# Kernel tuning notes

Measured on AMD Instinct MI355X. Metric: run time of the kernel, lower is better.

## Reference

```python
import jax, jax.numpy as jnp
import numpy as np

N, E, H = 40000, 640000, 128
EPS = 1e-5

def _bn(x, gamma, beta):
    # BatchNorm1d training-mode forward: batch mean / biased variance over axis 0
    mu = jnp.mean(x, axis=0)
    var = jnp.mean((x - mu) ** 2, axis=0)
    return (x - mu) * jax.lax.rsqrt(var + EPS) * gamma + beta


def setup_inputs() -> dict:
    key = jax.random.key(0)
    ks = jax.random.split(key, 12)
    s = 1.0 / np.sqrt(H)
    return {
        "x_feat": jax.random.normal(ks[0], (N, H), jnp.float32),
        "edge_attr": jax.random.normal(ks[1], (E, H), jnp.float32),
        "bases": jax.random.normal(ks[2], (E, H), jnp.float32),
        "src": jax.random.randint(ks[3], (E,), 0, N, jnp.int32),
        "dst": jax.random.randint(ks[4], (E,), 0, N, jnp.int32),
        "W1": jax.random.uniform(ks[5], (H, H), jnp.float32, -s, s),
        "b1": jnp.zeros((H,), jnp.float32),
        "W2": jax.random.uniform(ks[6], (H, H), jnp.float32, -s, s),
        "b2": jnp.zeros((H,), jnp.float32),
        "g1": jnp.ones((H,), jnp.float32),
        "be1": jnp.zeros((H,), jnp.float32),
        "W3": jax.random.uniform(ks[7], (H, H), jnp.float32, -s, s),
        "b3": jnp.zeros((H,), jnp.float32),
        "g2": jnp.ones((H,), jnp.float32),
        "be2": jnpp_zeros if False else jnp.zeros((H,), jnp.float32),
    }


def reference(x_feat, edge_attr, bases, src, dst,
              W1, b1, W2, b2, g1, be1, W3, b3, g2, be2):
    n_nodes = x_feat.shape[0]
    # edge gather-add: pos_e = x[src] + e
    pos_e = x_feat[src] + edge_attr                       # [E, H]
    # pre_ffn (Linear + exact GELU) then elementwise scale by bases
    v = jax.nn.gelu(pos_e @ W1.T + b1, approximate=False) * bases  # [E, H]
    # scatter-sum aggregation to destination nodes
    aggr = jax.ops.segment_sum(v, dst, num_segments=n_nodes)       # [N, H]
    # ffn: Linear -> BN -> GELU -> Linear -> BN -> GELU
    h = _bn(aggr @ W2.T + b2, g1, be1)
    h = jax.nn.gelu(h, approximate=False)
    h = _bn(h @ W3.T + b3, g2, be2)
    return jax.nn.gelu(h, approximate=False)
```

## Files before the change

### kernel.cpp

```cpp
#include <hip/hip_runtime.h>
#include <cmath>

#define H 128
#define EPS 1e-5f

typedef __attribute__((ext_vector_type(8))) __bf16 bf16x8;
typedef __attribute__((ext_vector_type(4))) float f32x4;
typedef __attribute__((ext_vector_type(2))) float f32x2;
typedef __attribute__((ext_vector_type(4))) unsigned short u16x4;
typedef __attribute__((ext_vector_type(8))) unsigned short u16x8;
typedef __attribute__((ext_vector_type(4))) int i32x4;

__device__ __forceinline__ float gelu_fast(float x) {
    float t2 = -1.5957691216057308f * fmaf(0.044715f * x * x, x, x);
    return x * __builtin_amdgcn_rcpf(1.0f + __expf(t2));
}

__device__ __forceinline__ unsigned short f2bfu(float f) {
    __bf16 h = (__bf16)f;
    return __builtin_bit_cast(unsigned short, h);
}

__global__ __launch_bounds__(256) void zero_kernel(int* __restrict__ p, int n4)
{
    int i = blockIdx.x * blockDim.x + threadIdx.x;
    const int stride = gridDim.x * blockDim.x;
    i32x4 z = {0, 0, 0, 0};
    for (; i < n4; i += stride)
        reinterpret_cast<i32x4*>(p)[i] = z;
}

__global__ __launch_bounds__(256) void hist_kernel(const int* __restrict__ dst,
                                                   int* __restrict__ cnt, int E)
{
    int i = blockIdx.x * blockDim.x + threadIdx.x;
    const int stride = gridDim.x * blockDim.x;
    for (; i < E; i += stride) atomicAdd(&cnt[dst[i]], 1);
}

__global__ __launch_bounds__(1024) void scan_kernel(const int* __restrict__ cnt,
                                                    int* __restrict__ offs,
                                                    int Nn, int E)
{
    __shared__ int part[1024];
    const int t = threadIdx.x;
    const int CH = (Nn + 1023) / 1024;
    const int base = t * CH;
    int s = 0;
    for (int i = 0; i < CH; ++i) {
        int idx = base + i;
        if (idx < Nn) s += cnt[idx];
    }
    part[t] = s;
    __syncthreads();
    for (int d = 1; d < 1024; d <<= 1) {
        int v = (t >= d) ? part[t - d] : 0;
        __syncthreads();
        part[t] += v;
        __syncthreads();
    }
    int run = (t > 0) ? part[t - 1] : 0;
    for (int i = 0; i < CH; ++i) {
        int idx = base + i;
        if (idx < Nn) {
            offs[idx] = run;
            run += cnt[idx];
        }
    }
    if (t == 0) offs[Nn] = E;
}

__global__ __launch_bounds__(256) void scatter_perm(const int* __restrict__ dst,
                                                    const int* __restrict__ offs,
                                                    int* __restrict__ cur2,
                                                    int* __restrict__ perm, int E)
{
    int i = blockIdx.x * blockDim.x + threadIdx.x;
    const int stride = gridDim.x * blockDim.x;
    for (; i < E; i += stride) {
        int n = dst[i];
        int p = offs[n] + atomicAdd(&cur2[n], 1);
        perm[p] = i;
    }
}

__global__ __launch_bounds__(256) void fused_edge(
    const float* __restrict__ x, const float* __restrict__ ea,
    const int* __restrict__ src, const float* __restrict__ W1,
    const float* __restrict__ b1, unsigned short* __restrict__ gbuf, int E)
{
    __shared__ __align__(16) unsigned short alds[64 * 128];

    const int tid = threadIdx.x;
    const int w = tid >> 6, l = tid & 63, lg = l >> 4, lr = l & 15;

    bf16x8 wf[2][4];
    f32x4 b1v[2];
#pragma unroll
    for (int ni = 0; ni < 2; ++ni) {
        int row = w * 32 + ni * 16 + lr;
#pragma unroll
        for (int kk = 0; kk < 4; ++kk) {
            const float* p = W1 + row * H + kk * 32 + lg * 8;
            u16x8 tt;
#pragma unroll
            for (int i = 0; i < 8; ++i) tt[i] = f2bfu(p[i]);
            wf[ni][kk] = __builtin_bit_cast(bf16x8, tt);
        }
        b1v[ni] = *reinterpret_cast<const f32x4*>(b1 + w * 32 + ni * 16 + lg * 4);
    }

    const int e0 = blockIdx.x * 64;

#pragma unroll
    for (int it = 0; it < 8; ++it) {
        const int gch = it * 256 + tid;
        const int row = gch >> 5;
        const int c16 = gch & 31;
        const int er = e0 + row;
        const int ec = er < E ? er : E - 1;
        const int s = src[ec];
        f32x4 a = *reinterpret_cast<const f32x4*>(ea + (long)ec * H + c16 * 4);
        f32x4 b = *reinterpret_cast<const f32x4*>(x + (long)s * H + c16 * 4);
        u16x4 o;
#pragma unroll
        for (int j = 0; j < 4; ++j) o[j] = f2bfu(a[j] + b[j]);
        const int col = c16 * 4;
        const int scol = col ^ ((row & 7) << 3);
        *reinterpret_cast<u16x4*>(&alds[row * 128 + scol]) = o;
    }
    __syncthreads();

#pragma unroll
    for (int s = 0; s < 4; ++s) {
        const int arow = s * 16 + lr;
        const int aswz = (arow & 7) << 3;
        bf16x8 af[4];
#pragma unroll
        for (int kk = 0; kk < 4; ++kk)
            af[kk] = __builtin_bit_cast(bf16x8,
                *reinterpret_cast<const u16x8*>(&alds[arow * 128 + ((kk * 32 + lg * 8) ^ aswz)]));
        const int es = e0 + s * 16 + lr;
#pragma unroll
        for (int ni = 0; ni < 2; ++ni) {
            f32x4 a4 = {0.f, 0.f, 0.f, 0.f};
#pragma unroll
            for (int kk = 0; kk < 4; ++kk)
                a4 = __builtin_amdgcn_mfma_f32_16x16x32_bf16(wf[ni][kk], af[kk], a4, 0, 0, 0);
            if (es < E) {
                u16x4 o;
#pragma unroll
                for (int r = 0; r < 4; ++r)
                    o[r] = f2bfu(gelu_fast(a4[r] + b1v[ni][r]));
                *reinterpret_cast<u16x4*>(gbuf + (size_t)es * H + w * 32 + ni * 16 + lg * 4) = o;
            }
        }
    }
}

__global__ __launch_bounds__(256) void aggregate_kernel(
    const unsigned short* __restrict__ gbuf, const float* __restrict__ bases,
    const int* __restrict__ perm, const int* __restrict__ offs,
    float* __restrict__ aggr, int Nn, int E)
{
    const int wv = threadIdx.x >> 6, lane = threadIdx.x & 63;
    const int n = blockIdx.x * 4 + wv;
    if (n >= Nn) return;
    const int lo = offs[n], hi = offs[n + 1];
    float a0 = 0.f, a1 = 0.f;
    int i = lo;
    for (; i + 3 < hi; i += 4) {
        int e0 = perm[i], e1 = perm[i + 1], e2 = perm[i + 2], e3 = perm[i + 3];
        e0 = (unsigned)e0 < (unsigned)E ? e0 : 0;
        e1 = (unsigned)e1 < (unsigned)E ? e1 : 0;
        e2 = (unsigned)e2 < (unsigned)E ? e2 : 0;
        e3 = (unsigned)e3 < (unsigned)E ? e3 : 0;
        unsigned u0 = *reinterpret_cast<const unsigned*>(gbuf + (size_t)e0 * H + lane * 2);
        unsigned u1 = *reinterpret_cast<const unsigned*>(gbuf + (size_t)e1 * H + lane * 2);
        unsigned u2 = *reinterpret_cast<const unsigned*>(gbuf + (size_t)e2 * H + lane * 2);
        unsigned u3 = *reinterpret_cast<const unsigned*>(gbuf + (size_t)e3 * H + lane * 2);
        f32x2 b0 = *reinterpret_cast<const f32x2*>(bases + (size_t)e0 * H + lane * 2);
        f32x2 b1_ = *reinterpret_cast<const f32x2*>(bases + (size_t)e1 * H + lane * 2);
        f32x2 b2 = *reinterpret_cast<const f32x2*>(bases + (size_t)e2 * H + lane * 2);
        f32x2 b3 = *reinterpret_cast<const f32x2*>(bases + (size_t)e3 * H + lane * 2);
        a0 += __builtin_bit_cast(float, u0 << 16) * b0[0]
            + __builtin_bit_cast(float, u1 << 16) * b1_[0]
            + __builtin_bit_cast(float, u2 << 16) * b2[0]
            + __builtin_bit_cast(float, u3 << 16) * b3[0];
        a1 += __builtin_bit_cast(float, u0 & 0xffff0000u) * b0[1]
            + __builtin_bit_cast(float, u1 & 0xffff0000u) * b1_[1]
            + __builtin_bit_cast(float, u2 & 0xffff0000u) * b2[1]
            + __builtin_bit_cast(float, u3 & 0xffff0000u) * b3[1];
    }
    for (; i < hi; ++i) {
        int e = perm[i];
        e = (unsigned)e < (unsigned)E ? e : 0;
        unsigned u0 = *reinterpret_cast<const unsigned*>(gbuf + (size_t)e * H + lane * 2);
        f32x2 b0 = *reinterpret_cast<const f32x2*>(bases + (size_t)e * H + lane * 2);
        a0 += __builtin_bit_cast(float, u0 << 16) * b0[0];
        a1 += __builtin_bit_cast(float, u0 & 0xffff0000u) * b0[1];
    }
    f32x2 o = {a0, a1};
    *reinterpret_cast<f32x2*>(aggr + (size_t)n * H + lane * 2) = o;
}

template <bool PRE>
__global__ __launch_bounds__(256) void node_gemm(
    const float* __restrict__ A, const float* __restrict__ W,
    const float* __restrict__ bias, const float* __restrict__ scl,
    const float* __restrict__ shf, float* __restrict__ Y,
    float* __restrict__ csum, float* __restrict__ cssq, int Nn)
{
    __shared__ __align__(16) unsigned short alds[64 * 128];

    const int tid = threadIdx.x;
    const int w = tid >> 6, l = tid & 63, lg = l >> 4, lr = l & 15;
    const int er = tid >> 2, q = tid & 3;
    const int r0 = blockIdx.x * 64;

    bf16x8 bf[2][4];
    float bv[2];
#pragma unroll
    for (int n = 0; n < 2; ++n) {
        int row = w * 32 + n * 16 + lr;
        bv[n] = bias[row];
#pragma unroll
        for (int kk = 0; kk < 4; ++kk) {
            const float* p = W + row * H + kk * 32 + lg * 8;
            u16x8 t;
#pragma unroll
            for (int i = 0; i < 8; ++i) t[i] = f2bfu(p[i]);
            bf[n][kk] = __builtin_bit_cast(bf16x8, t);
        }
    }

    {
        int rr = r0 + er;
        int rc = rr < Nn ? rr : Nn - 1;
        const f32x4* pa = reinterpret_cast<const f32x4*>(A + (long)rc * H + q * 32);
        const int swz = (er & 7) << 3;
#pragma unroll
        for (int i = 0; i < 8; ++i) {
            f32x4 v = pa[i];
            if constexpr (PRE) {
                f32x4 sc = *reinterpret_cast<const f32x4*>(scl + q * 32 + i * 4);
                f32x4 sh = *reinterpret_cast<const f32x4*>(shf + q * 32 + i * 4);
#pragma unroll
                for (int c = 0; c < 4; ++c) v[c] = gelu_fast(v[c] * sc[c] + sh[c]);
            }
            u16x4 o;
            o[0] = f2bfu(v[0]);
            o[1] = f2bfu(v[1]);
            o[2] = f2bfu(v[2]);
            o[3] = f2bfu(v[3]);
            int col = q * 32 + i * 4;
            *reinterpret_cast<u16x4*>(&alds[er * 128 + (col ^ swz)]) = o;
        }
    }
    __syncthreads();

    float ps[2] = {0.f, 0.f}, ps2[2] = {0.f, 0.f};
#pragma unroll
    for (int m = 0; m < 4; ++m) {
        const int arow = m * 16 + lr;
        const int aswz = (arow & 7) << 3;
        bf16x8 af[4];
#pragma unroll
        for (int kk = 0; kk < 4; ++kk)
            af[kk] = __builtin_bit_cast(bf16x8,
                *reinterpret_cast<const u16x8*>(&alds[arow * 128 + ((kk * 32 + lg * 8) ^ aswz)]));
#pragma unroll
        for (int n = 0; n < 2; ++n) {
            f32x4 a4 = {0.f, 0.f, 0.f, 0.f};
#pragma unroll
            for (int kk = 0; kk < 4; ++kk)
                a4 = __builtin_amdgcn_mfma_f32_16x16x32_bf16(af[kk], bf[n][kk], a4, 0, 0, 0);
            const int j = w * 32 + n * 16 + lr;
#pragma unroll
            for (int r = 0; r < 4; ++r) {
                int rr = r0 + m * 16 + lg * 4 + r;
                if (rr < Nn) {
                    float z = a4[r] + bv[n];
                    Y[(long)rr * H + j] = z;
                    ps[n] += z;
                    ps2[n] += z * z;
                }
            }
        }
    }
#pragma unroll
    for (int n = 0; n < 2; ++n) {
        float s = ps[n];
        s += __shfl_xor(s, 16);
        s += __shfl_xor(s, 32);
        float s2 = ps2[n];
        s2 += __shfl_xor(s2, 16);
        s2 += __shfl_xor(s2, 32);
        if (lg == 0) {
            int j = w * 32 + n * 16 + lr;
            atomicAdd(&csum[j], s);
            atomicAdd(&cssq[j], s2);
        }
    }
}

__global__ void finalize_bn(const float* __restrict__ csum, const float* __restrict__ cssq,
                            const float* __restrict__ g, const float* __restrict__ be,
                            float* __restrict__ scl, float* __restrict__ shf, float invN)
{
    int j = threadIdx.x;
    float mu = csum[j] * invN;
    float var = fmaxf(cssq[j] * invN - mu * mu, 0.f);
    float s = g[j] * rsqrtf(var + EPS);
    scl[j] = s;
    shf[j] = be[j] - mu * s;
}

__global__ __launch_bounds__(256) void final_gelu(
    const float* __restrict__ Y2, const float* __restrict__ scl,
    const float* __restrict__ shf, float* __restrict__ out, long n4)
{
    long i = (long)blockIdx.x * blockDim.x + threadIdx.x;
    const long stride = (long)gridDim.x * blockDim.x;
    for (; i < n4; i += stride) {
        f32x4 v = reinterpret_cast<const f32x4*>(Y2)[i];
        int c4 = (int)(i & 31);
        f32x4 sc = reinterpret_cast<const f32x4*>(scl)[c4];
        f32x4 sh = reinterpret_cast<const f32x4*>(shf)[c4];
        f32x4 o;
#pragma unroll
        for (int c = 0; c < 4; ++c) o[c] = gelu_fast(v[c] * sc[c] + sh[c]);
        reinterpret_cast<f32x4*>(out)[i] = o;
    }
}

extern "C" void kernel_launch(void* const* d_in, const int* in_sizes, int n_in,
                              void* d_out, int out_size, void* d_ws, size_t ws_size,
                              hipStream_t stream) {
    const float* x     = (const float*)d_in[0];
    const float* ea    = (const float*)d_in[1];
    const float* bases = (const float*)d_in[2];
    const int*   src   = (const int*)d_in[3];
    const int*   dst   = (const int*)d_in[4];
    const float* W1    = (const float*)d_in[5];
    const float* b1    = (const float*)d_in[6];
    const float* W2    = (const float*)d_in[7];
    const float* b2    = (const float*)d_in[8];
    const float* g1    = (const float*)d_in[9];
    const float* be1   = (const float*)d_in[10];
    const float* W3    = (const float*)d_in[11];
    const float* b3    = (const float*)d_in[12];
    const float* g2    = (const float*)d_in[13];
    const float* be2   = (const float*)d_in[14];

    const int N = in_sizes[0] / H;
    const int E = in_sizes[1] / H;

    float* ws    = (float*)d_ws;
    float* aggr  = ws;
    float* y1    = aggr + (size_t)N * H;
    float* stats = y1 + (size_t)N * H;
    float* sum1 = stats,        *ss1 = stats + 128;
    float* sum2 = stats + 256,  *ss2 = stats + 384;
    float* scl1 = stats + 512,  *shf1 = stats + 640;
    float* scl2 = stats + 768,  *shf2 = stats + 896;
    int* cnt  = (int*)(stats + 1024);
    int* cnt2 = cnt + N;
    int* perm = cnt2 + N;
    int* offs = perm + E;
    unsigned short* gbuf = (unsigned short*)(((uintptr_t)(offs + N + 1) + 4095) & ~(uintptr_t)4095);

    const int zn4 = (1024 + 2 * N + 3) / 4;
    zero_kernel<<<128, 256, 0, stream>>>((int*)stats, zn4);

    hist_kernel<<<2048, 256, 0, stream>>>(dst, cnt, E);
    scan_kernel<<<1, 1024, 0, stream>>>(cnt, offs, N, E);
    scatter_perm<<<2048, 256, 0, stream>>>(dst, offs, cnt2, perm, E);

    fused_edge<<<(E + 63) / 64, 256, 0, stream>>>(x, ea, src, W1, b1, gbuf, E);

    aggregate_kernel<<<(N + 3) / 4, 256, 0, stream>>>(gbuf, bases, perm, offs, aggr, N, E);

    const int nblk = (N + 63) / 64;
    node_gemm<false><<<nblk, 256, 0, stream>>>(aggr, W2, b2, nullptr, nullptr, y1, sum1, ss1, N);
    finalize_bn<<<1, 128, 0, stream>>>(sum1, ss1, g1, be1, scl1, shf1, 1.0f / (float)N);
    node_gemm<true><<<nblk, 256, 0, stream>>>(y1, W3, b3, scl1, shf1, aggr, sum2, ss2, N);
    finalize_bn<<<1, 128, 0, stream>>>(sum2, ss2, g2, be2, scl2, shf2, 1.0f / (float)N);

    long n4 = (long)N * H / 4;
    final_gelu<<<2048, 256, 0, stream>>>(aggr, scl2, shf2, (float*)d_out, n4);
}
```

Before: 471.3 us.

## Make fused_edge persistent with W1 staged once in LDS per block

The edge GEMM kernel becomes a persistent grid of 2048 blocks. Each block converts W1 to bf16 into swizzled LDS once, and each wave then loops independently over 16-edge tiles using a private LDS staging area, computing all 128 output columns. This removes the per-block reload and convert of W1 for every 64-edge tile and drops the block-wide barrier between the gather and the MFMA phases. In exchange, W1 fragments are now read from LDS on every MFMA instead of sitting in registers, and the wave-level gathers are smaller, which can reduce memory-level parallelism.

```diff
diff --git a/kernel.cpp b/kernel.cpp
--- a/kernel.cpp
+++ b/kernel.cpp
@@ -84,75 +84,83 @@
     }
 }
 
-__global__ __launch_bounds__(256) void fused_edge(
+__global__ __launch_bounds__(256, 3) void fused_edge(
     const float* __restrict__ x, const float* __restrict__ ea,
     const int* __restrict__ src, const float* __restrict__ W1,
-    const float* __restrict__ b1, unsigned short* __restrict__ gbuf, int E)
-{
-    __shared__ __align__(16) unsigned short alds[64 * 128];
+    const float* __restrict__ b1, unsigned short* __restrict__ gbuf,
+    int E, int ntiles)
+{
+    __shared__ __align__(16) unsigned short wlds[128 * 128];
+    __shared__ __align__(16) unsigned short tlds[4][16 * 128];
 
     const int tid = threadIdx.x;
     const int w = tid >> 6, l = tid & 63, lg = l >> 4, lr = l & 15;
 
-    bf16x8 wf[2][4];
-    f32x4 b1v[2];
-#pragma unroll
-    for (int ni = 0; ni < 2; ++ni) {
-        int row = w * 32 + ni * 16 + lr;
-#pragma unroll
-        for (int kk = 0; kk < 4; ++kk) {
-            const float* p = W1 + row * H + kk * 32 + lg * 8;
-            u16x8 tt;
-#pragma unroll
-            for (int i = 0; i < 8; ++i) tt[i] = f2bfu(p[i]);
-            wf[ni][kk] = __builtin_bit_cast(bf16x8, tt);
-        }
-        b1v[ni] = *reinterpret_cast<const f32x4*>(b1 + w * 32 + ni * 16 + lg * 4);
-    }
-
-    const int e0 = blockIdx.x * 64;
-
-#pragma unroll
-    for (int it = 0; it < 8; ++it) {
-        const int gch = it * 256 + tid;
-        const int row = gch >> 5;
-        const int c16 = gch & 31;
-        const int er = e0 + row;
-        const int ec = er < E ? er : E - 1;
-        const int s = src[ec];
-        f32x4 a = *reinterpret_cast<const f32x4*>(ea + (long)ec * H + c16 * 4);
-        f32x4 b = *reinterpret_cast<const f32x4*>(x + (long)s * H + c16 * 4);
+    for (int j = tid; j < 128 * 32; j += 256) {
+        const int row = j >> 5, c16 = j & 31;
+        f32x4 v = *reinterpret_cast<const f32x4*>(W1 + row * H + c16 * 4);
         u16x4 o;
 #pragma unroll
-        for (int j = 0; j < 4; ++j) o[j] = f2bfu(a[j] + b[j]);
+        for (int k = 0; k < 4; ++k) o[k] = f2bfu(v[k]);
         const int col = c16 * 4;
-        const int scol = col ^ ((row & 7) << 3);
-        *reinterpret_cast<u16x4*>(&alds[row * 128 + scol]) = o;
-    }
+        *reinterpret_cast<u16x4*>(&wlds[row * 128 + (col ^ ((row & 7) << 3))]) = o;
+    }
+    f32x4 b1v[8];
+#pragma unroll
+    for (int ni = 0; ni < 8; ++ni)
+        b1v[ni] = *reinterpret_cast<const f32x4*>(b1 + ni * 16 + lg * 4);
     __syncthreads();
 
-#pragma unroll
-    for (int s = 0; s < 4; ++s) {
-        const int arow = s * 16 + lr;
-        const int aswz = (arow & 7) << 3;
+    unsigned short* mylds = &tlds[w][0];
+    const int gw = blockIdx.x * 4 + w;
+    const int wstride = gridDim.x * 4;
+
+    for (int t = gw; t < ntiles; t += wstride) {
+        const int e0 = t * 16;
+
+#pragma unroll
+        for (int it = 0; it < 8; ++it) {
+            const int row = it * 2 + (l >> 5);
+            const int c16 = l & 31;
+            const int er = e0 + row;
+            const int ec = er < E ? er : E - 1;
+            const int s = src[ec];
+            f32x4 a = *reinterpret_cast<const f32x4*>(ea + (long)ec * H + c16 * 4);
+            f32x4 b = *reinterpret_cast<const f32x4*>(x + (long)s * H + c16 * 4);
+            u16x4 o;
+#pragma unroll
+            for (int j = 0; j < 4; ++j) o[j] = f2bfu(a[j] + b[j]);
+            const int col = c16 * 4;
+            *reinterpret_cast<u16x4*>(&mylds[row * 128 + (col ^ ((row & 7) << 3))]) = o;
+        }
+
+        const int aswz = (lr & 7) << 3;
         bf16x8 af[4];
 #pragma unroll
         for (int kk = 0; kk < 4; ++kk)
             af[kk] = __builtin_bit_cast(bf16x8,
-                *reinterpret_cast<const u16x8*>(&alds[arow * 128 + ((kk * 32 + lg * 8) ^ aswz)]));
-        const int es = e0 + s * 16 + lr;
-#pragma unroll
-        for (int ni = 0; ni < 2; ++ni) {
-            f32x4 a4 = {0.f, 0.f, 0.f, 0.f};
-#pragma unroll
-            for (int kk = 0; kk < 4; ++kk)
-                a4 = __builtin_amdgcn_mfma_f32_16x16x32_bf16(wf[ni][kk], af[kk], a4, 0, 0, 0);
-            if (es < E) {
+                *reinterpret_cast<const u16x8*>(&mylds[lr * 128 + ((kk * 32 + lg * 8) ^ aswz)]));
+
+        const int es = e0 + lr;
+        const bool ok = es < E;
+
+#pragma unroll
+        for (int ni = 0; ni < 8; ++ni) {
+            const int wrow = ni * 16 + lr;
+            const int wswz = (lr & 7) << 3;
+            f32x4 a4 = {b1v[ni][0], b1v[ni][1], b1v[ni][2], b1v[ni][3]};
+#pragma unroll
+            for (int kk = 0; kk < 4; ++kk) {
+                bf16x8 wf = __builtin_bit_cast(bf16x8,
+                    *reinterpret_cast<const u16x8*>(&wlds[wrow * 128 + ((kk * 32 + lg * 8) ^ wswz)]));
+                a4 = __builtin_amdgcn_mfma_f32_16x16x32_bf16(wf, af[kk], a4, 0, 0, 0);
+            }
+            if (ok) {
                 u16x4 o;
 #pragma unroll
                 for (int r = 0; r < 4; ++r)
-                    o[r] = f2bfu(gelu_fast(a4[r] + b1v[ni][r]));
-                *reinterpret_cast<u16x4*>(gbuf + (size_t)es * H + w * 32 + ni * 16 + lg * 4) = o;
+                    o[r] = f2bfu(gelu_fast(a4[r]));
+                *reinterpret_cast<u16x4*>(gbuf + (size_t)es * H + ni * 16 + lg * 4) = o;
             }
         }
     }
@@ -377,7 +385,8 @@
     scan_kernel<<<1, 1024, 0, stream>>>(cnt, offs, N, E);
     scatter_perm<<<2048, 256, 0, stream>>>(dst, offs, cnt2, perm, E);
 
-    fused_edge<<<(E + 63) / 64, 256, 0, stream>>>(x, ea, src, W1, b1, gbuf, E);
+    const int ntiles = (E + 15) / 16;
+    fused_edge<<<2048, 256, 0, stream>>>(x, ea, src, W1, b1, gbuf, E, ntiles);
 
     aggregate_kernel<<<(N + 3) / 4, 256, 0, stream>>>(gbuf, bases, perm, offs, aggr, N, E);
 
```

Result: slower. 575.3 us (+22.1%).

## Fuse edge GEMM with segmented scatter-sum via dst-sorted edges and atomics

Applied to the files above, without the earlier changes.

The edge MLP kernel now processes edges in dst-sorted order, multiplies by bases in-kernel, does a segmented shuffle reduction over runs of equal destination, and atomically adds run heads into aggr. This removes the bf16 intermediate gbuf round trip and the separate aggregate kernel. In exchange, the gathers of edge_attr and bases become indirect through perm, aggr needs an extra zeroing pass, and float atomics make the summation order nondeterministic. Bases are also rounded to bf16 before the multiply.

```diff
diff --git a/kernel.cpp b/kernel.cpp
--- a/kernel.cpp
+++ b/kernel.cpp
@@ -19,6 +19,10 @@
 __device__ __forceinline__ unsigned short f2bfu(float f) {
     __bf16 h = (__bf16)f;
     return __builtin_bit_cast(unsigned short, h);
+}
+
+__device__ __forceinline__ float bfu2f(unsigned short u) {
+    return __builtin_bit_cast(float, (unsigned)u << 16);
 }
 
 __global__ __launch_bounds__(256) void zero_kernel(int* __restrict__ p, int n4)
@@ -73,7 +77,8 @@
 __global__ __launch_bounds__(256) void scatter_perm(const int* __restrict__ dst,
                                                     const int* __restrict__ offs,
                                                     int* __restrict__ cur2,
-                                                    int* __restrict__ perm, int E)
+                                                    int* __restrict__ perm,
+                                                    int* __restrict__ dsts, int E)
 {
     int i = blockIdx.x * blockDim.x + threadIdx.x;
     const int stride = gridDim.x * blockDim.x;
@@ -81,15 +86,20 @@
         int n = dst[i];
         int p = offs[n] + atomicAdd(&cur2[n], 1);
         perm[p] = i;
-    }
-}
-
-__global__ __launch_bounds__(256) void fused_edge(
+        dsts[p] = n;
+    }
+}
+
+__global__ __launch_bounds__(256) void edge_aggr(
     const float* __restrict__ x, const float* __restrict__ ea,
-    const int* __restrict__ src, const float* __restrict__ W1,
-    const float* __restrict__ b1, unsigned short* __restrict__ gbuf, int E)
+    const float* __restrict__ bases, const int* __restrict__ src,
+    const int* __restrict__ perm, const int* __restrict__ dsts,
+    const float* __restrict__ W1, const float* __restrict__ b1,
+    float* __restrict__ aggr, int E)
 {
     __shared__ __align__(16) unsigned short alds[64 * 128];
+    __shared__ __align__(16) unsigned short blds[64 * 128];
+    __shared__ int nd_lds[64];
 
     const int tid = threadIdx.x;
     const int w = tid >> 6, l = tid & 63, lg = l >> 4, lr = l & 15;
@@ -111,26 +121,33 @@
     }
 
     const int e0 = blockIdx.x * 64;
+    if (tid < 64) {
+        int i = e0 + tid;
+        nd_lds[tid] = dsts[i < E ? i : E - 1];
+    }
 
 #pragma unroll
     for (int it = 0; it < 8; ++it) {
         const int gch = it * 256 + tid;
         const int row = gch >> 5;
         const int c16 = gch & 31;
-        const int er = e0 + row;
-        const int ec = er < E ? er : E - 1;
-        const int s = src[ec];
-        f32x4 a = *reinterpret_cast<const f32x4*>(ea + (long)ec * H + c16 * 4);
+        const int ip = e0 + row;
+        const int ic = ip < E ? ip : E - 1;
+        const int e = perm[ic];
+        const int s = src[e];
+        f32x4 a = *reinterpret_cast<const f32x4*>(ea + (long)e * H + c16 * 4);
         f32x4 b = *reinterpret_cast<const f32x4*>(x + (long)s * H + c16 * 4);
-        u16x4 o;
-#pragma unroll
-        for (int j = 0; j < 4; ++j) o[j] = f2bfu(a[j] + b[j]);
-        const int col = c16 * 4;
-        const int scol = col ^ ((row & 7) << 3);
+        f32x4 bs = *reinterpret_cast<const f32x4*>(bases + (long)e * H + c16 * 4);
+        u16x4 o, ob;
+#pragma unroll
+        for (int j = 0; j < 4; ++j) { o[j] = f2bfu(a[j] + b[j]); ob[j] = f2bfu(bs[j]); }
+        const int scol = (c16 * 4) ^ ((row & 7) << 3);
         *reinterpret_cast<u16x4*>(&alds[row * 128 + scol]) = o;
+        *reinterpret_cast<u16x4*>(&blds[row * 128 + scol]) = ob;
     }
     __syncthreads();
 
+    const int col0base = w * 32 + lg * 4;
 #pragma unroll
     for (int s = 0; s < 4; ++s) {
         const int arow = s * 16 + lr;
@@ -140,68 +157,44 @@
         for (int kk = 0; kk < 4; ++kk)
             af[kk] = __builtin_bit_cast(bf16x8,
                 *reinterpret_cast<const u16x8*>(&alds[arow * 128 + ((kk * 32 + lg * 8) ^ aswz)]));
-        const int es = e0 + s * 16 + lr;
+
+        const int es = e0 + arow;
+        const bool ok = es < E;
+        const int nd = nd_lds[arow];
+        const bool head = ok && (lr == 0 || nd != nd_lds[arow - 1]);
+
 #pragma unroll
         for (int ni = 0; ni < 2; ++ni) {
-            f32x4 a4 = {0.f, 0.f, 0.f, 0.f};
+            f32x4 a4 = b1v[ni];
 #pragma unroll
             for (int kk = 0; kk < 4; ++kk)
                 a4 = __builtin_amdgcn_mfma_f32_16x16x32_bf16(wf[ni][kk], af[kk], a4, 0, 0, 0);
-            if (es < E) {
-                u16x4 o;
-#pragma unroll
-                for (int r = 0; r < 4; ++r)
-                    o[r] = f2bfu(gelu_fast(a4[r] + b1v[ni][r]));
-                *reinterpret_cast<u16x4*>(gbuf + (size_t)es * H + w * 32 + ni * 16 + lg * 4) = o;
+
+            const int col0 = col0base + ni * 16;
+            u16x4 bq = *reinterpret_cast<const u16x4*>(&blds[arow * 128 + (col0 ^ aswz)]);
+            f32x4 v;
+#pragma unroll
+            for (int r = 0; r < 4; ++r)
+                v[r] = ok ? gelu_fast(a4[r]) * bfu2f(bq[r]) : 0.f;
+
+#pragma unroll
+            for (int d = 1; d < 16; d <<= 1) {
+                f32x4 vn;
+#pragma unroll
+                for (int r = 0; r < 4; ++r) vn[r] = __shfl_down(v[r], d);
+                int ndn = __shfl_down(nd, d);
+                bool take = (lr + d < 16) && (ndn == nd);
+#pragma unroll
+                for (int r = 0; r < 4; ++r) v[r] += take ? vn[r] : 0.f;
             }
-        }
-    }
-}
-
-__global__ __launch_bounds__(256) void aggregate_kernel(
-    const unsigned short* __restrict__ gbuf, const float* __restrict__ bases,
-    const int* __restrict__ perm, const int* __restrict__ offs,
-    float* __restrict__ aggr, int Nn, int E)
-{
-    const int wv = threadIdx.x >> 6, lane = threadIdx.x & 63;
-    const int n = blockIdx.x * 4 + wv;
-    if (n >= Nn) return;
-    const int lo = offs[n], hi = offs[n + 1];
-    float a0 = 0.f, a1 = 0.f;
-    int i = lo;
-    for (; i + 3 < hi; i += 4) {
-        int e0 = perm[i], e1 = perm[i + 1], e2 = perm[i + 2], e3 = perm[i + 3];
-        e0 = (unsigned)e0 < (unsigned)E ? e0 : 0;
-        e1 = (unsigned)e1 < (unsigned)E ? e1 : 0;
-        e2 = (unsigned)e2 < (unsigned)E ? e2 : 0;
-        e3 = (unsigned)e3 < (unsigned)E ? e3 : 0;
-        unsigned u0 = *reinterpret_cast<const unsigned*>(gbuf + (size_t)e0 * H + lane * 2);
-        unsigned u1 = *reinterpret_cast<const unsigned*>(gbuf + (size_t)e1 * H + lane * 2);
-        unsigned u2 = *reinterpret_cast<const unsigned*>(gbuf + (size_t)e2 * H + lane * 2);
-        unsigned u3 = *reinterpret_cast<const unsigned*>(gbuf + (size_t)e3 * H + lane * 2);
-        f32x2 b0 = *reinterpret_cast<const f32x2*>(bases + (size_t)e0 * H + lane * 2);
-        f32x2 b1_ = *reinterpret_cast<const f32x2*>(bases + (size_t)e1 * H + lane * 2);
-        f32x2 b2 = *reinterpret_cast<const f32x2*>(bases + (size_t)e2 * H + lane * 2);
-        f32x2 b3 = *reinterpret_cast<const f32x2*>(bases + (size_t)e3 * H + lane * 2);
-        a0 += __builtin_bit_cast(float, u0 << 16) * b0[0]
-            + __builtin_bit_cast(float, u1 << 16) * b1_[0]
-            + __builtin_bit_cast(float, u2 << 16) * b2[0]
-            + __builtin_bit_cast(float, u3 << 16) * b3[0];
-        a1 += __builtin_bit_cast(float, u0 & 0xffff0000u) * b0[1]
-            + __builtin_bit_cast(float, u1 & 0xffff0000u) * b1_[1]
-            + __builtin_bit_cast(float, u2 & 0xffff0000u) * b2[1]
-            + __builtin_bit_cast(float, u3 & 0xffff0000u) * b3[1];
-    }
-    for (; i < hi; ++i) {
-        int e = perm[i];
-        e = (unsigned)e < (unsigned)E ? e : 0;
-        unsigned u0 = *reinterpret_cast<const unsigned*>(gbuf + (size_t)e * H + lane * 2);
-        f32x2 b0 = *reinterpret_cast<const f32x2*>(bases + (size_t)e * H + lane * 2);
-        a0 += __builtin_bit_cast(float, u0 << 16) * b0[0];
-        a1 += __builtin_bit_cast(float, u0 & 0xffff0000u) * b0[1];
-    }
-    f32x2 o = {a0, a1};
-    *reinterpret_cast<f32x2*>(aggr + (size_t)n * H + lane * 2) = o;
+
+            if (head) {
+                float* dst = aggr + (long)nd * H + col0;
+#pragma unroll
+                for (int r = 0; r < 4; ++r) atomicAdd(&dst[r], v[r]);
+            }
+        }
+    }
 }
 
 template <bool PRE>
@@ -367,19 +360,19 @@
     int* cnt  = (int*)(stats + 1024);
     int* cnt2 = cnt + N;
     int* perm = cnt2 + N;
-    int* offs = perm + E;
-    unsigned short* gbuf = (unsigned short*)(((uintptr_t)(offs + N + 1) + 4095) & ~(uintptr_t)4095);
+    int* dsts = perm + E;
+    int* offs = dsts + E;
 
     const int zn4 = (1024 + 2 * N + 3) / 4;
     zero_kernel<<<128, 256, 0, stream>>>((int*)stats, zn4);
+    zero_kernel<<<1024, 256, 0, stream>>>((int*)aggr, N * H / 4);
 
     hist_kernel<<<2048, 256, 0, stream>>>(dst, cnt, E);
     scan_kernel<<<1, 1024, 0, stream>>>(cnt, offs, N, E);
-    scatter_perm<<<2048, 256, 0, stream>>>(dst, offs, cnt2, perm, E);
-
-    fused_edge<<<(E + 63) / 64, 256, 0, stream>>>(x, ea, src, W1, b1, gbuf, E);
-
-    aggregate_kernel<<<(N + 3) / 4, 256, 0, stream>>>(gbuf, bases, perm, offs, aggr, N, E);
+    scatter_perm<<<2048, 256, 0, stream>>>(dst, offs, cnt2, perm, dsts, E);
+
+    edge_aggr<<<(E + 63) / 64, 256, 0, stream>>>(x, ea, bases, src, perm, dsts,
+                                                 W1, b1, aggr, E);
 
     const int nblk = (N + 63) / 64;
     node_gemm<false><<<nblk, 256, 0, stream>>>(aggr, W2, b2, nullptr, nullptr, y1, sum1, ss1, N);
```

New measurement: 499.8 us. 6.1% more time.
